# Kernel tuning notes

Measured on AMD Instinct MI355X. Metric: run time of the kernel, lower is better.

Reference implementation:

```python
import jax, jax.numpy as jnp
import numpy as np

B, T, D_MODEL, D_K = 4, 4096, 1024, 64

def setup_inputs() -> dict:
    key = jax.random.key(0)
    k1, k2, k3, k4, k5 = jax.random.split(key, 5)
    x = jax.random.normal(k1, (B, T, D_MODEL), dtype=jnp.float32)
    # rotary freqs_cis as (real, imag) pairs: unit-magnitude like real RoPE
    theta = 10000.0
    inv = 1.0 / (theta ** (jnp.arange(0, D_K, 2, dtype=jnp.float32) / D_K))  # [D_K//2]
    ang = jnp.arange(T, dtype=jnp.float32)[:, None] * inv[None, :]           # [T, D_K//2]
    freqs_cis = jnp.stack([jnp.cos(ang), jnp.sin(ang)], axis=-1)             # [T, D_K//2, 2]
    scale = 1.0 / np.sqrt(D_MODEL)
    Wq = jax.random.normal(k2, (D_MODEL, D_K), dtype=jnp.float32) * scale
    Wk = jax.random.normal(k3, (D_MODEL, D_K), dtype=jnp.float32) * scale
    Wv = jax.random.normal(k4, (D_MODEL, D_K), dtype=jnp.float32) * scale
    return {"x": x, "freqs_cis": freqs_cis, "Wq": Wq, "Wk": Wk, "Wv": Wv}

def _apply_rope(t, fr, fi):
    # t: [B,T,D_K]; fr/fi: [T, D_K//2]. Complex mult on (even, odd) pairs.
    tp = t.reshape(*t.shape[:-1], D_K // 2, 2)       # [B,T,P,2]
    tr, ti = tp[..., 0], tp[..., 1]
    or_ = tr * fr - ti * fi
    oi_ = tr * fi + ti * fr
    return jnp.stack([or_, oi_], axis=-1).reshape(*t.shape[:-1], D_K)

def reference(x, freqs_cis, Wq, Wk, Wv):
    q = x @ Wq                                       # [B,T,D_K]
    k = x @ Wk
    v = x @ Wv
    fr, fi = freqs_cis[..., 0], freqs_cis[..., 1]    # [T, D_K//2]
    q = _apply_rope(q, fr, fi)
    k = _apply_rope(k, fr, fi)
    wei = jnp.einsum('btd,bsd->bts', q, k) * (D_K ** -0.5)   # [B,T,T]
    causal = jnp.tril(jnp.ones((T, T), dtype=bool))
    wei = jnp.where(causal, wei, -jnp.inf)
    wei = jax.nn.softmax(wei, axis=-1)
    return jnp.einsum('bts,bsd->btd', wei, v)        # [B,T,D_K]
```

## Files before the change

### kernel.cpp

```cpp
#include <hip/hip_runtime.h>
#include <hip/hip_bf16.h>

#define BB 4
#define TT 4096
#define DM 1024
#define DK 64
#define NSPLIT 8

using f32x4  = __attribute__((ext_vector_type(4))) float;
using bf16x8 = __attribute__((ext_vector_type(8))) short;

__device__ __forceinline__ short f2bf(float f) {
    __hip_bfloat16 h = __float2bfloat16(f);
    return __builtin_bit_cast(short, h);
}
__device__ __forceinline__ float bf2f(short s) {
    unsigned int u = ((unsigned int)(unsigned short)s) << 16;
    return __builtin_bit_cast(float, u);
}

__global__ __launch_bounds__(256) void wt_kernel(const float* __restrict__ Wq,
                                                 const float* __restrict__ Wk,
                                                 const float* __restrict__ Wv,
                                                 short* __restrict__ Wt) {
    int idx = blockIdx.x * 256 + threadIdx.x;
    if (idx >= 192 * 1024) return;
    int n = idx >> 10;
    int m = idx & 1023;
    const float* W = (n < 64) ? Wq : (n < 128) ? Wk : Wv;
    int c = n & 63;
    Wt[idx] = f2bf(W[m * 64 + c]);
}

__global__ __launch_bounds__(256, 6) void proj_rope(const float* __restrict__ x,
                                                    const float* __restrict__ freqs,
                                                    const short* __restrict__ Wt,
                                                    short* __restrict__ q,
                                                    short* __restrict__ k,
                                                    short* __restrict__ vt)
{
    __shared__ short As[2][2048];
    __shared__ short Bs[2][4096];

    int t  = threadIdx.x;
    int w  = t >> 6;
    int l  = t & 63;
    int lr = l & 15;
    int lg = (l >> 4) & 3;
    int wr = w & 1;
    int wc = w >> 1;
    int bx = blockIdx.x;
    int mt = (bx & 7) * 64 + (bx >> 3) / 3;
    int nh = (bx >> 3) % 3;
    int m0 = mt * 32;

    int arow = t >> 3, au = t & 7;
    int aswz = arow & 7;
    int brow = t >> 2, bu2 = (t & 3) * 2;
    int bswz = brow & 7;
    const float* gA = x  + (size_t)(m0 + arow) * DM + au * 8;
    const short* gB = Wt + (size_t)(nh * 64 + brow) * DM + bu2 * 8;

    f32x4 ar[2]; bf16x8 br[2];

#define LOADG(c_) do { int kk = (c_) << 6;                     \
        ar[0] = *(const f32x4*)(gA + kk);                      \
        ar[1] = *(const f32x4*)(gA + kk + 4);                  \
        br[0] = *(const bf16x8*)(gB + kk);                     \
        br[1] = *(const bf16x8*)(gB + kk + 8);                 \
    } while (0)

#define WRITELDS(buf_) do {                                                    \
        bf16x8 a0_;                                                            \
        for (int j_ = 0; j_ < 4; ++j_) {                                       \
            a0_[j_] = f2bf(ar[0][j_]); a0_[4 + j_] = f2bf(ar[1][j_]);          \
        }                                                                      \
        *(bf16x8*)&As[buf_][arow * 64 + ((au ^ aswz) << 3)] = a0_;             \
        *(bf16x8*)&Bs[buf_][brow * 64 + (((bu2    ) ^ bswz) << 3)] = br[0];    \
        *(bf16x8*)&Bs[buf_][brow * 64 + (((bu2 + 1) ^ bswz) << 3)] = br[1];    \
    } while (0)

    f32x4 acc[2];
#pragma unroll
    for (int i = 0; i < 2; ++i) acc[i] = (f32x4){0.f, 0.f, 0.f, 0.f};

    LOADG(0); WRITELDS(0); LOADG(1);
    __syncthreads();

    int cur = 0;
    int r7 = lr & 7;
    int amrow = (wr * 16 + lr) * 64;
    for (int ch = 0; ch < 16; ++ch) {
#pragma unroll
        for (int s = 0; s < 2; ++s) {
            int u0 = s * 4 + lg;
            bf16x8 af = *(const bf16x8*)&As[cur][amrow + ((u0 ^ r7) << 3)];
#pragma unroll
            for (int ntl = 0; ntl < 2; ++ntl) {
                int row = (wc * 2 + ntl) * 16 + lr;
                bf16x8 bfr = *(const bf16x8*)&Bs[cur][row * 64 + ((u0 ^ r7) << 3)];
                acc[ntl] = __builtin_amdgcn_mfma_f32_16x16x32_bf16(af, bfr, acc[ntl], 0, 0, 0);
            }
        }
        if (ch + 1 < 16) {
            WRITELDS(cur ^ 1);
            if (ch + 2 < 16) LOADG(ch + 2);
            __syncthreads();
            cur ^= 1;
        }
    }
#undef LOADG
#undef WRITELDS

    __syncthreads();

    if (nh == 2) {
        short* vs = &Bs[0][0];
#pragma unroll
        for (int r = 0; r < 4; ++r)
#pragma unroll
            for (int ntl = 0; ntl < 2; ++ntl)
                vs[(wr * 16 + lg * 4 + r) * 64 + (wc * 2 + ntl) * 16 + lr] = f2bf(acc[ntl][r]);
        __syncthreads();
        int b    = mt >> 7;
        int tt0  = (mt & 127) * 32;
        int c    = t >> 2;
        int tgrp = t & 3;
        bf16x8 v0;
#pragma unroll
        for (int j = 0; j < 8; ++j) v0[j] = vs[(tgrp * 8 + j) * 64 + c];
        *(bf16x8*)(vt + ((size_t)b * DK + c) * TT + tt0 + tgrp * 8) = v0;
    } else {
        short* dst = nh ? k : q;
        float postscale = nh ? 1.0f : 0.125f;
#pragma unroll
        for (int r = 0; r < 4; ++r) {
            int tg = m0 + wr * 16 + lg * 4 + r;
            int tt = tg & (TT - 1);
#pragma unroll
            for (int ntl = 0; ntl < 2; ++ntl) {
                int c = (wc * 2 + ntl) * 16 + lr;
                float e = acc[ntl][r];
                float p = __shfl_xor(e, 1);
                float2 f = ((const float2*)freqs)[(size_t)tt * 32 + (c >> 1)];
                float sgn = (c & 1) ? f.y : -f.y;
                dst[(size_t)tg * DK + c] = f2bf((e * f.x + p * sgn) * postscale);
            }
        }
    }
}

__global__ __launch_bounds__(256, 4) void attn_kernel(const short* __restrict__ q,
                                                      const short* __restrict__ k,
                                                      const short* __restrict__ vt,
                                                      short* __restrict__ po,
                                                      float* __restrict__ ml)
{
    __shared__ short Kb[64][64];
    __shared__ short Vb[64][64];
    __shared__ short pbuf[4][16][72];

    int w  = threadIdx.x >> 6;
    int l  = threadIdx.x & 63;
    int lr = l & 15;
    int lg = l >> 4;
    int b  = blockIdx.y;
    int s  = blockIdx.z;
    int qt = 63 - blockIdx.x;
    int q0 = qt * 64;
    int qrow_wave = q0 + w * 16;

    const short* qB = q  + (size_t)b * TT * DK;
    const short* kB = k  + (size_t)b * TT * DK;
    const short* vB = vt + (size_t)b * DK * TT;

    bf16x8 qf0 = *(const bf16x8*)(qB + (size_t)(qrow_wave + lr) * DK + 8 * lg);
    bf16x8 qf1 = *(const bf16x8*)(qB + (size_t)(qrow_wave + lr) * DK + 32 + 8 * lg);

    f32x4 of[4];
#pragma unroll
    for (int i = 0; i < 4; ++i) of[i] = (f32x4){0.f, 0.f, 0.f, 0.f};
    float m[4], lsum[4];
#pragma unroll
    for (int r = 0; r < 4; ++r) { m[r] = -INFINITY; lsum[r] = 0.f; }

    int nt = (qt >= s) ? ((qt - s + NSPLIT) >> 3) : 0;

    int srow = threadIdx.x >> 2;
    int u0   = (threadIdx.x & 3) * 2;
    int p0s  = ((u0) ^ (srow & 7)) * 8;
    int p1s  = ((u0 + 1) ^ (srow & 7)) * 8;

    bf16x8 kr0, kr1, vr0, vr1;
    short* mypb = &pbuf[w][0][0];

#define ISSUE(tile_) do {                                                        \
        int kv0_ = (tile_) << 6;                                                 \
        const short* gk_ = kB + (size_t)(kv0_ + srow) * DK + (u0 * 8);           \
        const short* gv_ = vB + (size_t)srow * TT + kv0_ + (u0 * 8);             \
        kr0 = *(const bf16x8*)gk_; kr1 = *(const bf16x8*)(gk_ + 8);              \
        vr0 = *(const bf16x8*)gv_; vr1 = *(const bf16x8*)(gv_ + 8);              \
    } while (0)

#define WRITE() do {                                                             \
        *(bf16x8*)&Kb[srow][p0s] = kr0;                                         \
        *(bf16x8*)&Kb[srow][p1s] = kr1;                                         \
        *(bf16x8*)&Vb[srow][p0s] = vr0;                                         \
        *(bf16x8*)&Vb[srow][p1s] = vr1;                                         \
    } while (0)

    if (nt > 0) {
        ISSUE(s); WRITE();
        if (nt > 1) ISSUE(s + NSPLIT);
        __syncthreads();
        for (int i = 0; i < nt; ++i) {
            int kv0 = (s + i * NSPLIT) << 6;

            f32x4 sc[4];
#pragma unroll
            for (int c = 0; c < 4; ++c) sc[c] = (f32x4){0.f, 0.f, 0.f, 0.f};
#pragma unroll
            for (int c = 0; c < 4; ++c) {
                int row = c * 16 + lr;
                bf16x8 kf0 = *(const bf16x8*)&Kb[row][((lg) ^ (row & 7)) * 8];
                bf16x8 kf1 = *(const bf16x8*)&Kb[row][((4 + lg) ^ (row & 7)) * 8];
                sc[c] = __builtin_amdgcn_mfma_f32_16x16x32_bf16(qf0, kf0, sc[c], 0, 0, 0);
                sc[c] = __builtin_amdgcn_mfma_f32_16x16x32_bf16(qf1, kf1, sc[c], 0, 0, 0);
            }

            if (kv0 == q0) {
#pragma unroll
                for (int r = 0; r < 4; ++r) {
                    int qg = qrow_wave + lg * 4 + r;
#pragma unroll
                    for (int c = 0; c < 4; ++c)
                        sc[c][r] = (kv0 + c * 16 + lr <= qg) ? sc[c][r] : -INFINITY;
                }
            }

            float mx[4];
#pragma unroll
            for (int r = 0; r < 4; ++r)
                mx[r] = fmaxf(fmaxf(sc[0][r], sc[1][r]), fmaxf(sc[2][r], sc[3][r]));
            bool needA = (mx[0] > m[0] + 8.f) || (mx[1] > m[1] + 8.f) ||
                         (mx[2] > m[2] + 8.f) || (mx[3] > m[3] + 8.f);
            if (__any(needA)) {
#pragma unroll
                for (int r = 0; r < 4; ++r) {
                    float t2 = mx[r];
                    t2 = fmaxf(t2, __shfl_xor(t2, 1));
                    t2 = fmaxf(t2, __shfl_xor(t2, 2));
                    t2 = fmaxf(t2, __shfl_xor(t2, 4));
                    t2 = fmaxf(t2, __shfl_xor(t2, 8));
                    float mn = fmaxf(m[r], t2);
                    float alpha = __expf(m[r] - mn);
                    m[r] = mn;
                    lsum[r] *= alpha;
#pragma unroll
                    for (int dt = 0; dt < 4; ++dt) of[dt][r] *= alpha;
                }
            }
#pragma unroll
            for (int r = 0; r < 4; ++r) {
                float p0 = __expf(sc[0][r] - m[r]);
                float p1 = __expf(sc[1][r] - m[r]);
                float p2 = __expf(sc[2][r] - m[r]);
                float p3 = __expf(sc[3][r] - m[r]);
                lsum[r] += (p0 + p1) + (p2 + p3);
                int prow = (lg * 4 + r) * 72;
                mypb[prow + lr]      = f2bf(p0);
                mypb[prow + 16 + lr] = f2bf(p1);
                mypb[prow + 32 + lr] = f2bf(p2);
                mypb[prow + 48 + lr] = f2bf(p3);
            }

#pragma unroll
            for (int ks = 0; ks < 2; ++ks) {
                bf16x8 pa = *(const bf16x8*)(mypb + lr * 72 + ks * 32 + 8 * lg);
#pragma unroll
                for (int dt = 0; dt < 4; ++dt) {
                    int row = dt * 16 + lr;
                    bf16x8 vf = *(const bf16x8*)&Vb[row][((ks * 4 + lg) ^ (row & 7)) * 8];
                    of[dt] = __builtin_amdgcn_mfma_f32_16x16x32_bf16(pa, vf, of[dt], 0, 0, 0);
                }
            }

            if (i + 1 < nt) {
                __syncthreads();
                WRITE();
                if (i + 2 < nt) ISSUE(s + (i + 2) * NSPLIT);
                __syncthreads();
            }
        }
    }
#undef ISSUE
#undef WRITE

#pragma unroll
    for (int r = 0; r < 4; ++r) {
        float ps = lsum[r];
        ps += __shfl_xor(ps, 1);
        ps += __shfl_xor(ps, 2);
        ps += __shfl_xor(ps, 4);
        ps += __shfl_xor(ps, 8);
        lsum[r] = ps;
    }

    short* myo  = po + (((size_t)b * 64 + qt) * NSPLIT + s) * 4096;
    float* myml = ml + (((size_t)b * 64 + qt) * NSPLIT + s) * 128;
#pragma unroll
    for (int r = 0; r < 4; ++r) {
        int row = w * 16 + lg * 4 + r;
#pragma unroll
        for (int dt = 0; dt < 4; ++dt) myo[row * 64 + dt * 16 + lr] = f2bf(of[dt][r]);
        if (lr == 0) { myml[row] = m[r]; myml[64 + row] = lsum[r]; }
    }
}

__global__ __launch_bounds__(256) void merge_kernel(const short* __restrict__ po,
                                                    const float* __restrict__ ml,
                                                    float* __restrict__ out)
{
    int qt = blockIdx.x;
    int b  = blockIdx.y;
    int row = threadIdx.x >> 2;
    int cg  = threadIdx.x & 3;

    size_t mlbase = ((size_t)b * 64 + qt) * NSPLIT * 128;
    float mm[NSPLIT], llv[NSPLIT];
#pragma unroll
    for (int s = 0; s < NSPLIT; ++s) {
        mm[s]  = ml[mlbase + s * 128 + row];
        llv[s] = ml[mlbase + s * 128 + 64 + row];
    }
    float M = -INFINITY;
#pragma unroll
    for (int s = 0; s < NSPLIT; ++s) M = fmaxf(M, mm[s]);
    float e[NSPLIT], den = 0.f;
#pragma unroll
    for (int s = 0; s < NSPLIT; ++s) { e[s] = __expf(mm[s] - M); den += e[s] * llv[s]; }
    float inv = 1.0f / den;

    size_t pbase = ((size_t)b * 64 + qt) * NSPLIT * 4096;
#pragma unroll
    for (int jj = 0; jj < 2; ++jj) {
        int col = cg * 16 + jj * 8;
        float acc8[8];
#pragma unroll
        for (int e2 = 0; e2 < 8; ++e2) acc8[e2] = 0.f;
#pragma unroll
        for (int s = 0; s < NSPLIT; ++s) {
            bf16x8 v = *(const bf16x8*)(po + pbase + s * 4096 + row * 64 + col);
#pragma unroll
            for (int e2 = 0; e2 < 8; ++e2) acc8[e2] += e[s] * bf2f(v[e2]);
        }
        float* orow = out + ((size_t)b * TT + qt * 64 + row) * DK + col;
#pragma unroll
        for (int e2 = 0; e2 < 8; ++e2) orow[e2] = acc8[e2] * inv;
    }
}

extern "C" void kernel_launch(void* const* d_in, const int* in_sizes, int n_in,
                              void* d_out, int out_size, void* d_ws, size_t ws_size,
                              hipStream_t stream) {
    const float* x     = (const float*)d_in[0];
    const float* freqs = (const float*)d_in[1];
    const float* Wq    = (const float*)d_in[2];
    const float* Wk    = (const float*)d_in[3];
    const float* Wv    = (const float*)d_in[4];
    float* out = (float*)d_out;

    char* ws = (char*)d_ws;
    short* Wt  = (short*)ws;
    short* qb  = (short*)(ws + 393216);
    short* kb  = (short*)(ws + 2490368);
    short* vtb = (short*)(ws + 4587520);
    short* po  = (short*)(ws + 6684672);
    float* ml  = (float*)(ws + 23461888);

    hipLaunchKernelGGL(wt_kernel, dim3(768), dim3(256), 0, stream, Wq, Wk, Wv, Wt);
    hipLaunchKernelGGL(proj_rope, dim3(1536), dim3(256), 0, stream, x, freqs, Wt, qb, kb, vtb);
    hipLaunchKernelGGL(attn_kernel, dim3(64, BB, NSPLIT), dim3(256), 0, stream, qb, kb, vtb, po, ml);
    hipLaunchKernelGGL(merge_kernel, dim3(64, BB), dim3(256), 0, stream, po, ml, out);
}
```

Baseline: 65.66 us.

## Compute Q, K and V projections in one block per row tile

Measured after the change: 60.92 us (median of 3 runs). 1.08x faster.

```diff
diff --git a/kernel.cpp b/kernel.cpp
--- a/kernel.cpp
+++ b/kernel.cpp
@@ -32,7 +32,7 @@
     Wt[idx] = f2bf(W[m * 64 + c]);
 }
 
-__global__ __launch_bounds__(256, 6) void proj_rope(const float* __restrict__ x,
+__global__ __launch_bounds__(256, 2) void proj_rope(const float* __restrict__ x,
                                                     const float* __restrict__ freqs,
                                                     const short* __restrict__ Wt,
                                                     short* __restrict__ q,
@@ -40,7 +40,7 @@
                                                     short* __restrict__ vt)
 {
     __shared__ short As[2][2048];
-    __shared__ short Bs[2][4096];
+    __shared__ short Bs[2][12288];
 
     int t  = threadIdx.x;
     int w  = t >> 6;
@@ -50,39 +50,40 @@
     int wr = w & 1;
     int wc = w >> 1;
     int bx = blockIdx.x;
-    int mt = (bx & 7) * 64 + (bx >> 3) / 3;
-    int nh = (bx >> 3) % 3;
+    int mt = (bx & 7) * 64 + (bx >> 3);
     int m0 = mt * 32;
 
     int arow = t >> 3, au = t & 7;
     int aswz = arow & 7;
-    int brow = t >> 2, bu2 = (t & 3) * 2;
-    int bswz = brow & 7;
+    int bswz = (t >> 3) & 7;
     const float* gA = x  + (size_t)(m0 + arow) * DM + au * 8;
-    const short* gB = Wt + (size_t)(nh * 64 + brow) * DM + bu2 * 8;
-
-    f32x4 ar[2]; bf16x8 br[2];
-
-#define LOADG(c_) do { int kk = (c_) << 6;                     \
-        ar[0] = *(const f32x4*)(gA + kk);                      \
-        ar[1] = *(const f32x4*)(gA + kk + 4);                  \
-        br[0] = *(const bf16x8*)(gB + kk);                     \
-        br[1] = *(const bf16x8*)(gB + kk + 8);                 \
+    const short* gB = Wt + (size_t)(t >> 3) * DM + (t & 7) * 8;
+
+    f32x4 ar[2]; bf16x8 br[6];
+
+#define LOADG(c_) do { int kk = (c_) << 6;                                      \
+        ar[0] = *(const f32x4*)(gA + kk);                                       \
+        ar[1] = *(const f32x4*)(gA + kk + 4);                                   \
+        _Pragma("unroll")                                                       \
+        for (int j_ = 0; j_ < 6; ++j_)                                          \
+            br[j_] = *(const bf16x8*)(gB + (size_t)(j_ * 32) * DM + kk);        \
     } while (0)
 
-#define WRITELDS(buf_) do {                                                    \
-        bf16x8 a0_;                                                            \
-        for (int j_ = 0; j_ < 4; ++j_) {                                       \
-            a0_[j_] = f2bf(ar[0][j_]); a0_[4 + j_] = f2bf(ar[1][j_]);          \
-        }                                                                      \
-        *(bf16x8*)&As[buf_][arow * 64 + ((au ^ aswz) << 3)] = a0_;             \
-        *(bf16x8*)&Bs[buf_][brow * 64 + (((bu2    ) ^ bswz) << 3)] = br[0];    \
-        *(bf16x8*)&Bs[buf_][brow * 64 + (((bu2 + 1) ^ bswz) << 3)] = br[1];    \
+#define WRITELDS(buf_) do {                                                     \
+        bf16x8 a0_;                                                             \
+        _Pragma("unroll")                                                       \
+        for (int j_ = 0; j_ < 4; ++j_) {                                        \
+            a0_[j_] = f2bf(ar[0][j_]); a0_[4 + j_] = f2bf(ar[1][j_]);           \
+        }                                                                       \
+        *(bf16x8*)&As[buf_][arow * 64 + ((au ^ aswz) << 3)] = a0_;              \
+        _Pragma("unroll")                                                       \
+        for (int j_ = 0; j_ < 6; ++j_)                                          \
+            *(bf16x8*)&Bs[buf_][(j_ * 32 + (t >> 3)) * 64 + (((t & 7) ^ bswz) << 3)] = br[j_]; \
     } while (0)
 
-    f32x4 acc[2];
-#pragma unroll
-    for (int i = 0; i < 2; ++i) acc[i] = (f32x4){0.f, 0.f, 0.f, 0.f};
+    f32x4 acc[6];
+#pragma unroll
+    for (int i = 0; i < 6; ++i) acc[i] = (f32x4){0.f, 0.f, 0.f, 0.f};
 
     LOADG(0); WRITELDS(0); LOADG(1);
     __syncthreads();
@@ -96,11 +97,13 @@
             int u0 = s * 4 + lg;
             bf16x8 af = *(const bf16x8*)&As[cur][amrow + ((u0 ^ r7) << 3)];
 #pragma unroll
-            for (int ntl = 0; ntl < 2; ++ntl) {
-                int row = (wc * 2 + ntl) * 16 + lr;
-                bf16x8 bfr = *(const bf16x8*)&Bs[cur][row * 64 + ((u0 ^ r7) << 3)];
-                acc[ntl] = __builtin_amdgcn_mfma_f32_16x16x32_bf16(af, bfr, acc[ntl], 0, 0, 0);
-            }
+            for (int nh = 0; nh < 3; ++nh)
+#pragma unroll
+                for (int ntl = 0; ntl < 2; ++ntl) {
+                    int row = nh * 64 + (wc * 2 + ntl) * 16 + lr;
+                    bf16x8 bfr = *(const bf16x8*)&Bs[cur][row * 64 + ((u0 ^ r7) << 3)];
+                    acc[nh * 2 + ntl] = __builtin_amdgcn_mfma_f32_16x16x32_bf16(af, bfr, acc[nh * 2 + ntl], 0, 0, 0);
+                }
         }
         if (ch + 1 < 16) {
             WRITELDS(cur ^ 1);
@@ -112,25 +115,8 @@
 #undef LOADG
 #undef WRITELDS
 
-    __syncthreads();
-
-    if (nh == 2) {
-        short* vs = &Bs[0][0];
-#pragma unroll
-        for (int r = 0; r < 4; ++r)
-#pragma unroll
-            for (int ntl = 0; ntl < 2; ++ntl)
-                vs[(wr * 16 + lg * 4 + r) * 64 + (wc * 2 + ntl) * 16 + lr] = f2bf(acc[ntl][r]);
-        __syncthreads();
-        int b    = mt >> 7;
-        int tt0  = (mt & 127) * 32;
-        int c    = t >> 2;
-        int tgrp = t & 3;
-        bf16x8 v0;
-#pragma unroll
-        for (int j = 0; j < 8; ++j) v0[j] = vs[(tgrp * 8 + j) * 64 + c];
-        *(bf16x8*)(vt + ((size_t)b * DK + c) * TT + tt0 + tgrp * 8) = v0;
-    } else {
+#pragma unroll
+    for (int nh = 0; nh < 2; ++nh) {
         short* dst = nh ? k : q;
         float postscale = nh ? 1.0f : 0.125f;
 #pragma unroll
@@ -139,8 +125,8 @@
             int tt = tg & (TT - 1);
 #pragma unroll
             for (int ntl = 0; ntl < 2; ++ntl) {
-                int c = (wc * 2 + ntl) * 16 + lr;
-                float e = acc[ntl][r];
+                int c = wc * 32 + ntl * 16 + lr;
+                float e = acc[nh * 2 + ntl][r];
                 float p = __shfl_xor(e, 1);
                 float2 f = ((const float2*)freqs)[(size_t)tt * 32 + (c >> 1)];
                 float sgn = (c & 1) ? f.y : -f.y;
@@ -148,6 +134,23 @@
             }
         }
     }
+
+    __syncthreads();
+    short* vs = &As[0][0];
+#pragma unroll
+    for (int r = 0; r < 4; ++r)
+#pragma unroll
+        for (int ntl = 0; ntl < 2; ++ntl)
+            vs[(wr * 16 + lg * 4 + r) * 64 + wc * 32 + ntl * 16 + lr] = f2bf(acc[4 + ntl][r]);
+    __syncthreads();
+    int b    = mt >> 7;
+    int tt0  = (mt & 127) * 32;
+    int c    = t >> 2;
+    int tgrp = t & 3;
+    bf16x8 v0;
+#pragma unroll
+    for (int j = 0; j < 8; ++j) v0[j] = vs[(tgrp * 8 + j) * 64 + c];
+    *(bf16x8*)(vt + ((size_t)b * DK + c) * TT + tt0 + tgrp * 8) = v0;
 }
 
 __global__ __launch_bounds__(256, 4) void attn_kernel(const short* __restrict__ q,
@@ -379,7 +382,7 @@
     float* ml  = (float*)(ws + 23461888);
 
     hipLaunchKernelGGL(wt_kernel, dim3(768), dim3(256), 0, stream, Wq, Wk, Wv, Wt);
-    hipLaunchKernelGGL(proj_rope, dim3(1536), dim3(256), 0, stream, x, freqs, Wt, qb, kb, vtb);
+    hipLaunchKernelGGL(proj_rope, dim3(512), dim3(256), 0, stream, x, freqs, Wt, qb, kb, vtb);
     hipLaunchKernelGGL(attn_kernel, dim3(64, BB, NSPLIT), dim3(256), 0, stream, qb, kb, vtb, po, ml);
     hipLaunchKernelGGL(merge_kernel, dim3(64, BB), dim3(256), 0, stream, po, ml, out);
 }
```
